# Kernel optimization log

Measured on AMD Instinct MI355X. Metric: run time of the kernel, lower is better.

The kernel has to match this reference:

```python
import jax, jax.numpy as jnp
import numpy as np

TEMPERATURE = 0.07
HARD_K = 10
N, D, NUM_CLASSES = 8192, 256, 128


def setup_inputs() -> dict:
    key = jax.random.key(0)
    kf, kl = jax.random.split(key)
    feats = jax.random.normal(kf, (N, D), dtype=jnp.float32)
    labels = jax.random.randint(kl, (N,), 0, NUM_CLASSES, dtype=jnp.int64)
    return {"feats": feats, "labels": labels}


def _loss(feats, labels):
    n = feats.shape[0]
    # F.normalize(dim=-1) with eps=1e-12
    norm = jnp.maximum(jnp.linalg.norm(feats, axis=-1, keepdims=True), 1e-12)
    z = feats / norm
    sim = (z @ z.T) / TEMPERATURE  # [N, N]

    same = labels[:, None] == labels[None, :]
    eye = jnp.eye(n, dtype=bool)
    same_ns = same & ~eye          # same label, excluding self
    diff = ~same                   # different label

    neg_inf = jnp.float32(-jnp.inf)
    # uniform random positive per row via Gumbel-max over the same-label mask
    g = jax.random.gumbel(jax.random.key(42), (n, n), dtype=jnp.float32)
    pos_idx = jnp.argmax(jnp.where(same_ns, g, neg_inf), axis=1)  # [N]
    pos_logit = jnp.take_along_axis(sim, pos_idx[:, None], axis=1)[:, 0]

    # hard negatives: top-k of sims over different-label columns
    neg_sims = jnp.where(diff, sim, neg_inf)
    hard_vals, _ = jax.lax.top_k(neg_sims, HARD_K)  # [N, K]; exp(-inf)=0 handles rows with <K negatives

    num = jnp.exp(pos_logit)
    den = num + jnp.sum(jnp.exp(hard_vals), axis=1)
    li = -jnp.log(jnp.maximum(num / jnp.maximum(den, 1e-8), 1e-8))

    valid = jnp.any(same_ns, axis=1) & jnp.any(diff, axis=1)
    cnt = jnp.maximum(jnp.sum(valid), 1)
    return jnp.sum(jnp.where(valid, li, 0.0)) / cnt.astype(li.dtype)


def reference(feats, labels):
    return _loss(feats, labels)
```

## Files before the change

kernel.cpp:

```cpp
#include <hip/hip_runtime.h>
#include <cstdint>
#include <math.h>

#define N_     8192
#define D_     256
#define NLBL   128
#define TEMP_INV 14.285714285714286f
#define HARDK  10
#define THETA  0.16f
#define GCAP   256

#define NCHUNK 32
#define CHUNK  (N_ / NCHUNK)
#define TILES  (CHUNK / 32)
#define CSLOT  16

typedef __attribute__((ext_vector_type(8)))  short bf16x8;
typedef __attribute__((ext_vector_type(16))) float f32x16;

__device__ __forceinline__ uint32_t rotl32(uint32_t x, int n) {
  return (x << n) | (x >> (32 - n));
}
__device__ uint32_t tf_bits(uint32_t idx) {
  uint32_t x0 = 0u, x1 = idx;
  const uint32_t k0 = 0u, k1 = 42u;
  const uint32_t k2 = k0 ^ k1 ^ 0x1BD11BDAu;
  x0 += k0; x1 += k1;
#define TFR(r) { x0 += x1; x1 = rotl32(x1, r); x1 ^= x0; }
  TFR(13) TFR(15) TFR(26) TFR(6)
  x0 += k1; x1 += k2 + 1u;
  TFR(17) TFR(29) TFR(16) TFR(24)
  x0 += k2; x1 += k0 + 2u;
  TFR(13) TFR(15) TFR(26) TFR(6)
  x0 += k0; x1 += k1 + 3u;
  TFR(17) TFR(29) TFR(16) TFR(24)
  x0 += k1; x1 += k2 + 4u;
  TFR(13) TFR(15) TFR(26) TFR(6)
  x0 += k2; x1 += k0 + 5u;
#undef TFR
  return x0 ^ x1;
}

__device__ __forceinline__ uint32_t f2bf(float x) {
  uint32_t b = __float_as_uint(x);
  return (b + 0x7FFFu + ((b >> 16) & 1u)) >> 16;
}

__global__ __launch_bounds__(256) void prep_group_kernel(
    const float* __restrict__ feats, const int* __restrict__ labels,
    float* __restrict__ inv_norm, unsigned short* __restrict__ zt,
    uint32_t* __restrict__ mask_g, int* __restrict__ glist, int* __restrict__ cnt_g) {
  __shared__ uint4 tile[16][33];
  __shared__ int lcnt;
  const int tid = threadIdx.x;

  if (blockIdx.x < 512) {
    const int row0 = blockIdx.x * 16;
    const int wv = tid >> 6, l = tid & 63;
#pragma unroll
    for (int rr = 0; rr < 4; ++rr) {
      const int rloc = wv * 4 + rr;
      const int row = row0 + rloc;
      float4 v = ((const float4*)feats)[(size_t)row * 64 + l];
      float ss = v.x * v.x + v.y * v.y + v.z * v.z + v.w * v.w;
#pragma unroll
      for (int o = 32; o; o >>= 1) ss += __shfl_xor(ss, o);
      float inv = 1.0f / fmaxf(sqrtf(ss), 1e-12f);
      if (l == 0) inv_norm[row] = inv;
      uint2 p;
      p.x = f2bf(v.x * inv) | (f2bf(v.y * inv) << 16);
      p.y = f2bf(v.z * inv) | (f2bf(v.w * inv) << 16);
      *(uint2*)((char*)&tile[0][0] + rloc * 528 + l * 8) = p;
    }
    __syncthreads();
#pragma unroll
    for (int it = 0; it < 2; ++it) {
      int idx = it * 256 + tid;
      int c = idx >> 4, r = idx & 15;
      ((uint4*)zt)[(size_t)c * N_ + row0 + r] = tile[r][c];
    }
  } else {
    const int b = blockIdx.x - 512;
    const int lane = tid & 63, wv = tid >> 6;
    if (tid == 0) lcnt = 0;
    __syncthreads();
    for (int it = 0; it < N_; it += 256) {
      int col = it + tid;
      bool pred = (labels[col] == b);
      unsigned long long m = __ballot(pred);
      if (lane == 0) {
        int w0 = (it + wv * 64) >> 5;
        mask_g[b * 256 + w0]     = (uint32_t)m;
        mask_g[b * 256 + w0 + 1] = (uint32_t)(m >> 32);
      }
      if (pred) {
        int p = atomicAdd(&lcnt, 1);
        if (p < GCAP) glist[b * GCAP + p] = col;
      }
    }
    __syncthreads();
    if (tid == 0) cnt_g[b] = lcnt;
  }
}

__device__ __forceinline__ void stage_tile(const unsigned short* zt, char (*AbK)[1024],
                                           int colT, int wid, int l, int kg) {
  const char* base = (const char*)zt + ((size_t)kg * N_ + colT + (l & 31)) * 16;
#pragma unroll
  for (int q = 0; q < 2; ++q) {
    const int kk = wid * 2 + q;
    __builtin_amdgcn_global_load_lds(
        (const __attribute__((address_space(1))) void*)(base + (size_t)kk * (2 * N_ * 16)),
        (__attribute__((address_space(3))) void*)(&AbK[kk][0]), 16, 0, 0);
  }
}

#define INS8(H0,H1,H2,H3,H4,H5,H6,H7,POS,C) \
  { H0 = (POS==0)?(C):H0; H1 = (POS==1)?(C):H1; H2 = (POS==2)?(C):H2; H3 = (POS==3)?(C):H3; \
    H4 = (POS==4)?(C):H4; H5 = (POS==5)?(C):H5; H6 = (POS==6)?(C):H6; H7 = (POS==7)?(C):H7; \
    ++POS; }

__global__ __launch_bounds__(512) void collect_kernel(const unsigned short* __restrict__ zt,
                                                      const int* __restrict__ labels,
                                                      const uint32_t* __restrict__ mask_g,
                                                      float* __restrict__ vals,
                                                      int* __restrict__ counts) {
  __shared__ char Ab[2][16][1024];
  __shared__ float mcell[256 * 2 * 8];
  __shared__ int   mcnt[256 * 2];

  const int tid = threadIdx.x;
  const int l = tid & 63, wid = tid >> 6;
  const int kg = l >> 5;

  int rc = 0, rem = blockIdx.x;
  while (rem >= NCHUNK - rc) { rem -= NCHUNK - rc; ++rc; }
  const int cc = rc + rem;
  const bool offdiag = (cc > rc);

  const int row0 = rc * 256;
  const int col0 = cc * CHUNK;
  const int rowW = row0 + wid * 32 + (l & 31);
  const int lab = labels[rowW];

  mcnt[tid] = 0;

  uint32_t mW[TILES];
  {
    const uint4* mm = (const uint4*)(mask_g + lab * 256 + (col0 >> 5));
    uint4 m0 = mm[0], m1 = mm[1];
    mW[0]=m0.x; mW[1]=m0.y; mW[2]=m0.z; mW[3]=m0.w;
    mW[4]=m1.x; mW[5]=m1.y; mW[6]=m1.z; mW[7]=m1.w;
  }

  bf16x8 bf[16];
  {
    const uint4* ztq = (const uint4*)zt;
#pragma unroll
    for (int kk = 0; kk < 16; ++kk)
      bf[kk] = *(const bf16x8*)&ztq[(size_t)(kk * 2 + kg) * N_ + rowW];
  }

  float h0=0,h1=0,h2=0,h3=0,h4=0,h5=0,h6=0,h7=0;
  int pos = 0;
  float* vb = vals + ((size_t)rowW * NCHUNK + cc) * CSLOT + kg * 8;
  const int mhalf = (rowW >> 2) & 1;

  stage_tile(zt, Ab[0], col0, wid, l, kg);
  __syncthreads();

  int buf = 0;
#pragma unroll
  for (int t = 0; t < TILES; ++t) {
    if (t + 1 < TILES) stage_tile(zt, Ab[buf ^ 1], col0 + (t + 1) * 32, wid, l, kg);

    f32x16 acc;
#pragma unroll
    for (int r = 0; r < 16; ++r) acc[r] = 0.f;
    __builtin_amdgcn_s_setprio(1);
#pragma unroll
    for (int kk = 0; kk < 16; ++kk) {
      bf16x8 a = *(const bf16x8*)&Ab[buf][kk][l * 16];
      acc = __builtin_amdgcn_mfma_f32_32x32x16_bf16(a, bf[kk], acc, 0, 0, 0);
    }
    __builtin_amdgcn_s_setprio(0);

    const uint32_t wsh = mW[t] >> (kg * 4);
#pragma unroll
    for (int r = 0; r < 16; ++r) {
      const int cpos = (r & 3) + 8 * (r >> 2);
      bool hit = ((((wsh >> cpos) & 1u) == 0u) && (acc[r] > THETA));
      if (__any(hit)) {
        if (hit) {
          INS8(h0,h1,h2,h3,h4,h5,h6,h7, pos, acc[r]);
          if (offdiag) {
            int jc = t * 32 + cpos + 4 * kg;
            int p = atomicAdd(&mcnt[jc * 2 + mhalf], 1);
            if (p < 8) mcell[(jc * 2 + mhalf) * 8 + p] = acc[r];
          }
        }
      }
    }
    __syncthreads();
    buf ^= 1;
  }

  {
    float4 a0 = {h0, h1, h2, h3};
    float4 a1 = {h4, h5, h6, h7};
    *(float4*)(vb)     = a0;
    *(float4*)(vb + 4) = a1;
    counts[(rowW * NCHUNK + cc) * 2 + kg] = pos;
  }

  if (offdiag) {
    int jc = tid >> 1, half = tid & 1;
    int cnt = mcnt[jc * 2 + half];
    float4 m0 = *(float4*)&mcell[(jc * 2 + half) * 8];
    float4 m1 = *(float4*)&mcell[(jc * 2 + half) * 8 + 4];
    float* dm = vals + ((size_t)(col0 + jc) * NCHUNK + rc) * CSLOT + half * 8;
    *(float4*)(dm)     = m0;
    *(float4*)(dm + 4) = m1;
    counts[((col0 + jc) * NCHUNK + rc) * 2 + half] = cnt;
  }
}

__global__ __launch_bounds__(256) void finalize_kernel(
    const float* __restrict__ feats, const int* __restrict__ labels,
    const float* __restrict__ inv_norm,
    const int* __restrict__ glist, const int* __restrict__ cnt_g,
    const int* __restrict__ counts, const float* __restrict__ vals,
    float* __restrict__ li, int* __restrict__ valid) {
  const int row = blockIdx.x * 4 + (threadIdx.x >> 6);
  const int lane = threadIdx.x & 63;
  const int lab = labels[row];
  const int gc = cnt_g[lab];
  const int gn = gc < GCAP ? gc : GCAP;
  const float4* feats4 = (const float4*)feats;

  uint32_t bk = 0u; int bj = -1;
  for (int e = lane; e < gn; e += 64) {
    int j = glist[lab * GCAP + e];
    if (j != row) {
      uint32_t key = tf_bits((uint32_t)row * (uint32_t)N_ + (uint32_t)j) >> 9;
      if (bj < 0 || key > bk || (key == bk && j < bj)) { bk = key; bj = j; }
    }
  }
#pragma unroll
  for (int o = 32; o; o >>= 1) {
    uint32_t ok = __shfl_xor(bk, o);
    int oj = __shfl_xor(bj, o);
    if (oj >= 0 && (bj < 0 || ok > bk || (ok == bk && oj < bj))) { bk = ok; bj = oj; }
  }

  float pc = 0.f;
  if (bj >= 0) {
    float4 a = feats4[(size_t)row * 64 + lane];
    float4 b = feats4[(size_t)bj * 64 + lane];
    float p = a.x * b.x + a.y * b.y + a.z * b.z + a.w * b.w;
#pragma unroll
    for (int o = 32; o; o >>= 1) p += __shfl_xor(p, o);
    pc = p * inv_norm[row] * inv_norm[bj];
  }

  float vv[8];
  int ovf = 0;
#pragma unroll
  for (int q = 0; q < 8; ++q) {
    int s = lane + 64 * q;
    int cell = s >> 4, wi = s & 15;
    int c0 = counts[(row * NCHUNK + cell) * 2 + 0];
    int c1 = counts[(row * NCHUNK + cell) * 2 + 1];
    ovf |= ((c0 > 8) || (c1 > 8)) ? 1 : 0;
    float val = vals[(size_t)row * (NCHUNK * CSLOT) + s];
    bool live = (wi < 8) ? (wi < c0) : ((wi - 8) < c1);
    vv[q] = live ? val : -INFINITY;
  }

  float num = expf(pc * TEMP_INV);
  float den = num;
  int got = 0;
#pragma unroll 1
  for (int it = 0; it < HARDK; ++it) {
    float lm = fmaxf(fmaxf(fmaxf(vv[0], vv[1]), fmaxf(vv[2], vv[3])),
                     fmaxf(fmaxf(vv[4], vv[5]), fmaxf(vv[6], vv[7])));
    float wm = lm;
#pragma unroll
    for (int o = 32; o; o >>= 1) wm = fmaxf(wm, __shfl_xor(wm, o));
    if (wm < -1e37f) break;
    den += expf(wm * TEMP_INV);
    ++got;
    unsigned long long b = __ballot(lm == wm);
    int fl = __ffsll((long long)b) - 1;
    if (lane == fl) {
      if      (vv[0] == wm) vv[0] = -INFINITY;
      else if (vv[1] == wm) vv[1] = -INFINITY;
      else if (vv[2] == wm) vv[2] = -INFINITY;
      else if (vv[3] == wm) vv[3] = -INFINITY;
      else if (vv[4] == wm) vv[4] = -INFINITY;
      else if (vv[5] == wm) vv[5] = -INFINITY;
      else if (vv[6] == wm) vv[6] = -INFINITY;
      else                  vv[7] = -INFINITY;
    }
  }

  const int ndiff = N_ - gc;
  const bool vld = (bj >= 0) && (ndiff > 0);
  const int want = ndiff < HARDK ? ndiff : HARDK;

  if (vld && (__any(ovf) || got < want)) {
    float tk[HARDK];
#pragma unroll
    for (int k = 0; k < HARDK; ++k) tk[k] = -INFINITY;
    const float invr = inv_norm[row];
    const float4 a = feats4[(size_t)row * 64 + lane];
#pragma unroll 1
    for (int j = 0; j < N_; ++j) {
      if (j == row || labels[j] == lab) continue;
      float4 b = feats4[(size_t)j * 64 + lane];
      float p = a.x * b.x + a.y * b.y + a.z * b.z + a.w * b.w;
#pragma unroll
      for (int o = 32; o; o >>= 1) p += __shfl_xor(p, o);
      float c = p * invr * inv_norm[j];
      if (c > tk[0]) {
        tk[0] = c;
#pragma unroll
        for (int q = 0; q < HARDK - 1; ++q)
          if (tk[q] > tk[q + 1]) { float tmp = tk[q]; tk[q] = tk[q + 1]; tk[q + 1] = tmp; }
      }
    }
    den = num;
#pragma unroll
    for (int k = 0; k < HARDK; ++k)
      if (tk[k] > -1e37f) den += expf(tk[k] * TEMP_INV);
  }

  float L = 0.f;
  if (vld) L = -logf(fmaxf(num / fmaxf(den, 1e-8f), 1e-8f));
  if (lane == 0) {
    li[row] = L;
    valid[row] = vld ? 1 : 0;
  }
}

__global__ __launch_bounds__(256) void reduce_kernel(const float* __restrict__ li,
                                                     const int* __restrict__ valid,
                                                     float* __restrict__ out) {
  __shared__ float ssum[4];
  __shared__ int scnt[4];
  float s = 0.f; int c = 0;
  for (int i = threadIdx.x; i < N_; i += 256) { s += li[i]; c += valid[i]; }
#pragma unroll
  for (int o = 32; o; o >>= 1) { s += __shfl_down(s, o); c += __shfl_down(c, o); }
  if ((threadIdx.x & 63) == 0) { ssum[threadIdx.x >> 6] = s; scnt[threadIdx.x >> 6] = c; }
  __syncthreads();
  if (threadIdx.x == 0) {
    float S = 0.f; int C = 0;
    for (int w = 0; w < 4; ++w) { S += ssum[w]; C += scnt[w]; }
    out[0] = S / (float)(C > 0 ? C : 1);
  }
}

extern "C" void kernel_launch(void* const* d_in, const int* in_sizes, int n_in,
                              void* d_out, int out_size, void* d_ws, size_t ws_size,
                              hipStream_t stream) {
  const float* feats  = (const float*)d_in[0];
  const int*   labels = (const int*)d_in[1];
  float* out = (float*)d_out;

  char* w = (char*)d_ws;
  unsigned short* zt  = (unsigned short*)w;  w += (size_t)N_ * D_ * 2;
  float* inv_norm = (float*)w;               w += (size_t)N_ * 4;
  uint32_t* mask_g = (uint32_t*)w;           w += (size_t)NLBL * 256 * 4;
  int* glist = (int*)w;                      w += (size_t)NLBL * GCAP * 4;
  int* cnt_g = (int*)w;                      w += (size_t)NLBL * 4;
  int* counts = (int*)w;                     w += (size_t)N_ * NCHUNK * 2 * 4;
  float* vals = (float*)w;                   w += (size_t)N_ * NCHUNK * CSLOT * 4;
  float* li_arr = (float*)w;                 w += (size_t)N_ * 4;
  int* valid_arr = (int*)w;                  w += (size_t)N_ * 4;

  hipLaunchKernelGGL(prep_group_kernel, dim3(640), dim3(256), 0, stream,
                     feats, labels, inv_norm, zt, mask_g, glist, cnt_g);
  hipLaunchKernelGGL(collect_kernel, dim3((NCHUNK * (NCHUNK + 1)) / 2), dim3(512), 0, stream,
                     zt, labels, mask_g, vals, counts);
  hipLaunchKernelGGL(finalize_kernel, dim3(N_ / 4), dim3(256), 0, stream,
                     feats, labels, inv_norm, glist, cnt_g, counts, vals, li_arr, valid_arr);
  hipLaunchKernelGGL(reduce_kernel, dim3(1), dim3(256), 0, stream, li_arr, valid_arr, out);
}
```

Before: 92.51 us.

## Halve collect tile to 128x128 blocks and pack candidate slots to eight per cell

The collect kernel now uses 64 chunks with 128-row by 128-column blocks of 256 threads, giving 2080 blocks instead of 528 for better load balance over the triangular grid. Per-cell candidate storage shrinks from 16 to 8 slots. The two half-wave lists are written from opposite ends of the slot, and finalize reconstructs liveness from both counts. Mirrored off-diagonal writes use a single 8-slot list per column. Smaller blocks reduce per-block data reuse and raise the chance of overflow, which falls back to a slow path.

```diff
diff --git a/kernel.cpp b/kernel.cpp
--- a/kernel.cpp
+++ b/kernel.cpp
@@ -10,10 +10,10 @@
 #define THETA  0.16f
 #define GCAP   256
 
-#define NCHUNK 32
+#define NCHUNK 64
 #define CHUNK  (N_ / NCHUNK)
 #define TILES  (CHUNK / 32)
-#define CSLOT  16
+#define CSLOT  8
 
 typedef __attribute__((ext_vector_type(8)))  short bf16x8;
 typedef __attribute__((ext_vector_type(16))) float f32x16;
@@ -107,8 +107,8 @@
                                            int colT, int wid, int l, int kg) {
   const char* base = (const char*)zt + ((size_t)kg * N_ + colT + (l & 31)) * 16;
 #pragma unroll
-  for (int q = 0; q < 2; ++q) {
-    const int kk = wid * 2 + q;
+  for (int q = 0; q < 4; ++q) {
+    const int kk = wid * 4 + q;
     __builtin_amdgcn_global_load_lds(
         (const __attribute__((address_space(1))) void*)(base + (size_t)kk * (2 * N_ * 16)),
         (__attribute__((address_space(3))) void*)(&AbK[kk][0]), 16, 0, 0);
@@ -120,14 +120,14 @@
     H4 = (POS==4)?(C):H4; H5 = (POS==5)?(C):H5; H6 = (POS==6)?(C):H6; H7 = (POS==7)?(C):H7; \
     ++POS; }
 
-__global__ __launch_bounds__(512) void collect_kernel(const unsigned short* __restrict__ zt,
+__global__ __launch_bounds__(256) void collect_kernel(const unsigned short* __restrict__ zt,
                                                       const int* __restrict__ labels,
                                                       const uint32_t* __restrict__ mask_g,
                                                       float* __restrict__ vals,
                                                       int* __restrict__ counts) {
   __shared__ char Ab[2][16][1024];
-  __shared__ float mcell[256 * 2 * 8];
-  __shared__ int   mcnt[256 * 2];
+  __shared__ float mcell[128 * 8];
+  __shared__ int   mcnt[128];
 
   const int tid = threadIdx.x;
   const int l = tid & 63, wid = tid >> 6;
@@ -138,19 +138,17 @@
   const int cc = rc + rem;
   const bool offdiag = (cc > rc);
 
-  const int row0 = rc * 256;
+  const int row0 = rc * 128;
   const int col0 = cc * CHUNK;
   const int rowW = row0 + wid * 32 + (l & 31);
   const int lab = labels[rowW];
 
-  mcnt[tid] = 0;
+  if (tid < 128) mcnt[tid] = 0;
 
   uint32_t mW[TILES];
   {
-    const uint4* mm = (const uint4*)(mask_g + lab * 256 + (col0 >> 5));
-    uint4 m0 = mm[0], m1 = mm[1];
-    mW[0]=m0.x; mW[1]=m0.y; mW[2]=m0.z; mW[3]=m0.w;
-    mW[4]=m1.x; mW[5]=m1.y; mW[6]=m1.z; mW[7]=m1.w;
+    uint4 m0 = *(const uint4*)(mask_g + lab * 256 + (col0 >> 5));
+    mW[0] = m0.x; mW[1] = m0.y; mW[2] = m0.z; mW[3] = m0.w;
   }
 
   bf16x8 bf[16];
@@ -163,8 +161,7 @@
 
   float h0=0,h1=0,h2=0,h3=0,h4=0,h5=0,h6=0,h7=0;
   int pos = 0;
-  float* vb = vals + ((size_t)rowW * NCHUNK + cc) * CSLOT + kg * 8;
-  const int mhalf = (rowW >> 2) & 1;
+  float* vb = vals + ((size_t)rowW * NCHUNK + cc) * CSLOT;
 
   stage_tile(zt, Ab[0], col0, wid, l, kg);
   __syncthreads();
@@ -195,8 +192,8 @@
           INS8(h0,h1,h2,h3,h4,h5,h6,h7, pos, acc[r]);
           if (offdiag) {
             int jc = t * 32 + cpos + 4 * kg;
-            int p = atomicAdd(&mcnt[jc * 2 + mhalf], 1);
-            if (p < 8) mcell[(jc * 2 + mhalf) * 8 + p] = acc[r];
+            int p = atomicAdd(&mcnt[jc], 1);
+            if (p < 8) mcell[jc * 8 + p] = acc[r];
           }
         }
       }
@@ -205,23 +202,28 @@
     buf ^= 1;
   }
 
-  {
-    float4 a0 = {h0, h1, h2, h3};
-    float4 a1 = {h4, h5, h6, h7};
-    *(float4*)(vb)     = a0;
-    *(float4*)(vb + 4) = a1;
-    counts[(rowW * NCHUNK + cc) * 2 + kg] = pos;
-  }
+  if (kg == 0) {
+    if (pos > 0) vb[0] = h0;  if (pos > 1) vb[1] = h1;
+    if (pos > 2) vb[2] = h2;  if (pos > 3) vb[3] = h3;
+    if (pos > 4) vb[4] = h4;  if (pos > 5) vb[5] = h5;
+    if (pos > 6) vb[6] = h6;  if (pos > 7) vb[7] = h7;
+  } else {
+    if (pos > 0) vb[7] = h0;  if (pos > 1) vb[6] = h1;
+    if (pos > 2) vb[5] = h2;  if (pos > 3) vb[4] = h3;
+    if (pos > 4) vb[3] = h4;  if (pos > 5) vb[2] = h5;
+    if (pos > 6) vb[1] = h6;  if (pos > 7) vb[0] = h7;
+  }
+  counts[(rowW * NCHUNK + cc) * 2 + kg] = pos;
 
   if (offdiag) {
     int jc = tid >> 1, half = tid & 1;
-    int cnt = mcnt[jc * 2 + half];
-    float4 m0 = *(float4*)&mcell[(jc * 2 + half) * 8];
-    float4 m1 = *(float4*)&mcell[(jc * 2 + half) * 8 + 4];
-    float* dm = vals + ((size_t)(col0 + jc) * NCHUNK + rc) * CSLOT + half * 8;
-    *(float4*)(dm)     = m0;
-    *(float4*)(dm + 4) = m1;
-    counts[((col0 + jc) * NCHUNK + rc) * 2 + half] = cnt;
+    float4 m = *(float4*)&mcell[jc * 8 + half * 4];
+    float* dm = vals + ((size_t)(col0 + jc) * NCHUNK + rc) * CSLOT + half * 4;
+    *(float4*)dm = m;
+    if (half == 0) {
+      counts[((col0 + jc) * NCHUNK + rc) * 2 + 0] = mcnt[jc];
+      counts[((col0 + jc) * NCHUNK + rc) * 2 + 1] = 0;
+    }
   }
 }
 
@@ -268,12 +270,13 @@
 #pragma unroll
   for (int q = 0; q < 8; ++q) {
     int s = lane + 64 * q;
-    int cell = s >> 4, wi = s & 15;
+    int cell = s >> 3, wi = s & 7;
     int c0 = counts[(row * NCHUNK + cell) * 2 + 0];
     int c1 = counts[(row * NCHUNK + cell) * 2 + 1];
-    ovf |= ((c0 > 8) || (c1 > 8)) ? 1 : 0;
+    ovf |= (c0 + c1 > CSLOT) ? 1 : 0;
     float val = vals[(size_t)row * (NCHUNK * CSLOT) + s];
-    bool live = (wi < 8) ? (wi < c0) : ((wi - 8) < c1);
+    int c1b = c1 < CSLOT ? c1 : CSLOT;
+    bool live = (wi < c0) || (wi >= CSLOT - c1b);
     vv[q] = live ? val : -INFINITY;
   }
 
@@ -381,7 +384,7 @@
 
   hipLaunchKernelGGL(prep_group_kernel, dim3(640), dim3(256), 0, stream,
                      feats, labels, inv_norm, zt, mask_g, glist, cnt_g);
-  hipLaunchKernelGGL(collect_kernel, dim3((NCHUNK * (NCHUNK + 1)) / 2), dim3(512), 0, stream,
+  hipLaunchKernelGGL(collect_kernel, dim3((NCHUNK * (NCHUNK + 1)) / 2), dim3(256), 0, stream,
                      zt, labels, mask_g, vals, counts);
   hipLaunchKernelGGL(finalize_kernel, dim3(N_ / 4), dim3(256), 0, stream,
                      feats, labels, inv_norm, glist, cnt_g, counts, vals, li_arr, valid_arr);
```

Measured after the change: 85.20 us. -7.9%, faster.
